# Optimization experiments

Measured on AMD Instinct MI355X. Metric: run time of the kernel, lower is better.

The kernel has to match this reference:

```python
import jax, jax.numpy as jnp
import numpy as np

N_NODES = 50000
N_EDGES = 800000
IN_FEAT = 128
HID = 128
OUT = 10
N_GRAPHS = 128
BN_EPS = 1e-5


def setup_inputs() -> dict:
    key = jax.random.key(0)
    ks = jax.random.split(key, 16)
    inp = {
        "n_feat": jax.random.normal(ks[0], (N_NODES, IN_FEAT), dtype=jnp.float32),
        "src": jax.random.randint(ks[1], (N_EDGES,), 0, N_NODES),
        "dst": jax.random.randint(ks[2], (N_EDGES,), 0, N_NODES),
        "graph_ids": jnp.sort(jax.random.randint(ks[3], (N_NODES,), 0, N_GRAPHS)),
        # GraphConv weights (DGL layout: weight [in, out], bias [out])
        "W1": jax.random.normal(ks[4], (IN_FEAT, HID), dtype=jnp.float32) / np.sqrt(IN_FEAT),
        "b1": jnp.zeros((HID,), dtype=jnp.float32),
        "W2": jax.random.normal(ks[5], (HID, HID), dtype=jnp.float32) / np.sqrt(HID),
        "b2": jnp.zeros((HID,), dtype=jnp.float32),
        # BatchNorm1d affine params
        "gamma": jnp.ones((HID,), dtype=jnp.float32),
        "beta": jnp.zeros((HID,), dtype=jnp.float32),
        # MLP head
        "fc1_w": jax.random.normal(ks[6], (HID, HID), dtype=jnp.float32) / np.sqrt(HID),
        "fc1_b": jnp.zeros((HID,), dtype=jnp.float32),
        "fc2_w": jax.random.normal(ks[7], (HID, OUT), dtype=jnp.float32) / np.sqrt(HID),
        "fc2_b": jnp.zeros((OUT,), dtype=jnp.float32),
    }
    return inp


def _graph_conv(x, W, b, src, dst, inv_sqrt_out, inv_sqrt_in):
    # DGL GraphConv, norm='both': h = D_in^{-1/2} A D_out^{-1/2} x W + b
    h = x * inv_sqrt_out[:, None]          # [N, d_in]
    h = h @ W                              # [N, d_out] (project before gather: fewer bytes moved)
    agg = jax.ops.segment_sum(h[src], dst, num_segments=N_NODES)  # gather + scatter-add
    return agg * inv_sqrt_in[:, None] + b


def reference(n_feat, src, dst, graph_ids, W1, b1, W2, b2, gamma, beta,
              fc1_w, fc1_b, fc2_w, fc2_b):
    ones_e = jnp.ones((N_EDGES,), dtype=jnp.float32)
    deg_out = jnp.clip(jax.ops.segment_sum(ones_e, src, num_segments=N_NODES), 1.0)
    deg_in = jnp.clip(jax.ops.segment_sum(ones_e, dst, num_segments=N_NODES), 1.0)
    inv_sqrt_out = jax.lax.rsqrt(deg_out)
    inv_sqrt_in = jax.lax.rsqrt(deg_in)

    x = jax.nn.relu(_graph_conv(n_feat, W1, b1, src, dst, inv_sqrt_out, inv_sqrt_in))
    # dropout is identity in eval mode
    x = jax.nn.relu(_graph_conv(x, W2, b2, src, dst, inv_sqrt_out, inv_sqrt_in))

    # SumPooling over graphs
    embedding = jax.ops.segment_sum(x, graph_ids, num_segments=N_GRAPHS)  # [B, HID]

    # BatchNorm1d (training-mode batch stats, biased variance like torch)
    mu = jnp.mean(embedding, axis=0)
    var = jnp.mean(jnp.square(embedding - mu), axis=0)
    h = gamma * (embedding - mu) * jax.lax.rsqrt(var + BN_EPS) + beta

    h = jax.nn.relu(h @ fc1_w + fc1_b)
    logits = h @ fc2_w + fc2_b
    return embedding, jax.nn.log_softmax(logits, axis=-1)
```

## Files before the change

kernel.cpp:

```cpp
#include <hip/hip_runtime.h>
#include <hip/hip_bf16.h>
#include <math.h>

#define N_NODES 50000
#define N_EDGES 800000
#define HID 128
#define N_GRAPHS 128
#define OUTC 10
#define BN_EPS 1e-5f

#define SCAN_B 256
#define N_SCAN_BLOCKS ((N_NODES + SCAN_B - 1) / SCAN_B)

#define HB 128
#define HW8 (N_NODES / 4)
#define HR_B 256
#define HR_BLOCKS ((HW8 + HR_B - 1) / HR_B)

#define EPAD 8
#define E_SRC_CAP (N_EDGES + N_NODES * EPAD)

#define LDA 136
#define LDAF 132

#define MM_BLOCKS ((N_NODES + 64) / 64)

#define AGG_NODES 16
#define AGG_BLOCKS (N_NODES / AGG_NODES)

#define PSLOTS 3

typedef short short8 __attribute__((ext_vector_type(8)));
typedef float floatx4 __attribute__((ext_vector_type(4)));

template <typename T, typename F>
__device__ inline T bitcast(F f) {
    union { F a; T b; } u;
    u.a = f;
    return u.b;
}

__device__ inline unsigned short f2bf(float x) {
    return __hip_bfloat16_raw(__float2bfloat16(x)).x;
}

__global__ __launch_bounds__(1024) void hist_part_kernel(const int* __restrict__ src,
                                                         const int* __restrict__ dst,
                                                         unsigned int* __restrict__ part,
                                                         const float* __restrict__ W1,
                                                         const float* __restrict__ W2,
                                                         unsigned short* __restrict__ Wp) {
    if (blockIdx.x == 2 * HB) {
        for (int q = threadIdx.x; q < 4096; q += 1024) {
            int wi = q >> 11;
            const float* __restrict__ W = wi ? W2 : W1;
            int t2 = q & 2047;
            int tile = t2 >> 6, lane = t2 & 63;
            int kc = tile >> 3, nt = tile & 7;
            int n = lane & 15, quad = lane >> 4;
            unsigned short v[8];
#pragma unroll
            for (int j = 0; j < 8; j++) {
                int k = kc * 32 + quad * 8 + j;
                v[j] = f2bf(W[k * HID + nt * 16 + n]);
            }
            *(uint4*)&Wp[(size_t)q * 8] = *(uint4*)v;
        }
        return;
    }
    __shared__ unsigned int h[HW8];
    for (int i = threadIdx.x; i < HW8; i += 1024) h[i] = 0;
    __syncthreads();
    int half = (blockIdx.x >= HB) ? 1 : 0;
    const int* __restrict__ idx = half ? dst : src;
    int b = blockIdx.x - half * HB;
    for (int e = b * 1024 + threadIdx.x; e < N_EDGES; e += HB * 1024) {
        int v = idx[e];
        atomicAdd(&h[v >> 2], 1u << ((v & 3) << 3));
    }
    __syncthreads();
    unsigned int* __restrict__ out = part + (size_t)blockIdx.x * HW8;
    for (int i = threadIdx.x; i < HW8; i += 1024) out[i] = h[i];
}

__global__ __launch_bounds__(HR_B) void hist_reduce_kernel(unsigned int* __restrict__ part,
                                                           int* __restrict__ cnt_in,
                                                           float* __restrict__ inv_out,
                                                           float* __restrict__ inv_in,
                                                           int* __restrict__ bsum) {
    int t = threadIdx.x;
    int w = blockIdx.x * HR_B + t;
    int padsum = 0;
    if (w < HW8) {
        unsigned int s = 0, d = 0;
        for (int b = 0; b < HB; b++) {
            s += part[(size_t)b * HW8 + w];
            unsigned int c = part[(size_t)(b + HB) * HW8 + w];
            part[(size_t)(b + HB) * HW8 + w] = d;
            d += c;
        }
#pragma unroll
        for (int j = 0; j < 4; j++) {
            int i = w * 4 + j;
            int so = (int)((s >> (j * 8)) & 0xFFu);
            int di = (int)((d >> (j * 8)) & 0xFFu);
            cnt_in[i] = di;
            inv_out[i] = rsqrtf(fmaxf((float)so, 1.0f));
            inv_in[i] = rsqrtf(fmaxf((float)di, 1.0f));
            padsum += (di + EPAD - 1) & ~(EPAD - 1);
        }
    }
#pragma unroll
    for (int o = 32; o > 0; o >>= 1) padsum += __shfl_xor(padsum, o);
    if ((t & 63) == 0) bsum[blockIdx.x * 4 + (t >> 6)] = padsum;
}

__device__ inline void mm_tail(const unsigned short* __restrict__ xs,
                               const unsigned short* __restrict__ Wp,
                               __hip_bfloat16* __restrict__ Y, int row0) {
    int tid = threadIdx.x;
    int wave = tid >> 6, lane = tid & 63;
    int m = lane & 15, quad = lane >> 4;
    int rowl = wave * 16;

    short8 a[4];
#pragma unroll
    for (int kc = 0; kc < 4; kc++)
        a[kc] = bitcast<short8>(*(const uint4*)&xs[(rowl + m) * LDA + kc * 32 + quad * 8]);

    floatx4 acc[8];
#pragma unroll
    for (int nt = 0; nt < 8; nt++) acc[nt] = (floatx4){0.f, 0.f, 0.f, 0.f};

#pragma unroll
    for (int nt = 0; nt < 8; nt++) {
#pragma unroll
        for (int kc = 0; kc < 4; kc++) {
            short8 bfr = bitcast<short8>(
                *(const uint4*)&Wp[((size_t)(kc * 8 + nt) * 64 + lane) * 8]);
            acc[nt] = __builtin_amdgcn_mfma_f32_16x16x32_bf16(a[kc], bfr, acc[nt], 0, 0, 0);
        }
    }

#pragma unroll
    for (int nt = 0; nt < 8; nt++) {
#pragma unroll
        for (int i = 0; i < 4; i++) {
            int rg = row0 + rowl + quad * 4 + i;
            if (rg < N_NODES + 1) {
                Y[(size_t)rg * HID + nt * 16 + m] = __float2bfloat16(acc[nt][i]);
            }
        }
    }
}

__global__ __launch_bounds__(256) void scanmm1_kernel(const int* __restrict__ cnt,
                                                      const int* __restrict__ bsum,
                                                      int* __restrict__ row_ptr,
                                                      int* __restrict__ edge_src,
                                                      const float* __restrict__ X,
                                                      const float* __restrict__ scale,
                                                      const unsigned short* __restrict__ Wp,
                                                      __hip_bfloat16* __restrict__ Y,
                                                      __hip_bfloat16* __restrict__ Y2,
                                                      float* __restrict__ emb) {
    __shared__ unsigned short xs[64 * LDA];
    int t = threadIdx.x;
    int b = blockIdx.x;

    if (b >= N_SCAN_BLOCKS) {
        if (b == N_SCAN_BLOCKS + MM_BLOCKS) {
            for (int i = t; i < N_GRAPHS * HID; i += 256) emb[i] = 0.f;
            if (t < 16) {
                uint4 z = make_uint4(0u, 0u, 0u, 0u);
                *(uint4*)&Y2[(size_t)N_NODES * HID + t * 8] = z;
            }
            return;
        }
        int row0 = (b - N_SCAN_BLOCKS) * 64;
        for (int j = 0; j < 8; j++) {
            int idx4 = j * 256 + t;
            int r = idx4 >> 5;
            int col = (idx4 & 31) * 4;
            int rg = row0 + r;
            float4 v = make_float4(0.f, 0.f, 0.f, 0.f);
            if (rg < N_NODES) {
                v = *(const float4*)&X[(size_t)rg * HID + col];
                float sc = scale[rg];
                v.x *= sc; v.y *= sc; v.z *= sc; v.w *= sc;
            }
            unsigned short o[4];
            o[0] = f2bf(v.x); o[1] = f2bf(v.y); o[2] = f2bf(v.z); o[3] = f2bf(v.w);
            *(ushort4*)&xs[r * LDA + col] = *(ushort4*)o;
        }
        __syncthreads();
        mm_tail(xs, Wp, Y, row0);
        return;
    }

    int* sb = (int*)xs;
    int* part = (int*)xs + 256;
    sb[t] = (t < N_SCAN_BLOCKS) ? bsum[t] : 0;
    __syncthreads();
    for (int off = 1; off < SCAN_B; off <<= 1) {
        int u = (t >= off) ? sb[t - off] : 0;
        __syncthreads();
        sb[t] += u;
        __syncthreads();
    }
    int boff = (b == 0) ? 0 : sb[b - 1];

    int i = b * SCAN_B + t;
    int raw = (i < N_NODES) ? cnt[i] : 0;
    int v = (raw + EPAD - 1) & ~(EPAD - 1);
    part[t] = v;
    __syncthreads();
    for (int off = 1; off < SCAN_B; off <<= 1) {
        int u = (t >= off) ? part[t - off] : 0;
        __syncthreads();
        part[t] += u;
        __syncthreads();
    }
    if (i < N_NODES) {
        int ex = part[t] - v + boff;
        row_ptr[i] = ex;
        for (int p = ex + raw; p < ex + v; p++) edge_src[p] = N_NODES;
        if (i == N_NODES - 1) row_ptr[N_NODES] = ex + v;
    }
}

__global__ __launch_bounds__(1024) void csr_fill_kernel(const int* __restrict__ src,
                                                        const int* __restrict__ dst,
                                                        const unsigned int* __restrict__ part,
                                                        const int* __restrict__ row_ptr,
                                                        int* __restrict__ edge_src) {
    __shared__ unsigned int loc[HW8];
    int b = blockIdx.x;
    const unsigned int* __restrict__ off = part + (size_t)(b + HB) * HW8;
    for (int i = threadIdx.x; i < HW8; i += 1024) loc[i] = off[i];
    __syncthreads();
    for (int e = b * 1024 + threadIdx.x; e < N_EDGES; e += HB * 1024) {
        int d = dst[e];
        unsigned int old = atomicAdd(&loc[d >> 2], 1u << ((d & 3) << 3));
        int local = (int)((old >> ((d & 3) << 3)) & 0xFFu);
        edge_src[row_ptr[d] + local] = src[e];
    }
}

#define ACC8(u)                                                                              \
    acc[0] += __uint_as_float(u.x << 16); acc[1] += __uint_as_float(u.x & 0xFFFF0000u);      \
    acc[2] += __uint_as_float(u.y << 16); acc[3] += __uint_as_float(u.y & 0xFFFF0000u);      \
    acc[4] += __uint_as_float(u.z << 16); acc[5] += __uint_as_float(u.z & 0xFFFF0000u);      \
    acc[6] += __uint_as_float(u.w << 16); acc[7] += __uint_as_float(u.w & 0xFFFF0000u);

#define GATHER_CONT(idxv)                                                                    \
    for (int j = 16; j < mm0; j += 8) {                                                      \
        int s0 = __shfl(idxv, j + esub);                                                     \
        int s1 = __shfl(idxv, j + 4 + esub);                                                 \
        uint4 u0 = Yq[s0 * (HID / 8) + f16];                                                 \
        uint4 u1 = Yq[s1 * (HID / 8) + f16];                                                 \
        ACC8(u0); ACC8(u1);                                                                  \
    }

#define GATHER_BODY(idxv)                                                                    \
    {                                                                                        \
        int j = 0;                                                                           \
        for (; j + 16 <= mm; j += 16) {                                                      \
            int s0 = __shfl(idxv, j + esub);                                                 \
            int s1 = __shfl(idxv, j + 4 + esub);                                             \
            int s2 = __shfl(idxv, j + 8 + esub);                                             \
            int s3 = __shfl(idxv, j + 12 + esub);                                            \
            uint4 u0 = Yq[s0 * (HID / 8) + f16];                                             \
            uint4 u1 = Yq[s1 * (HID / 8) + f16];                                             \
            uint4 u2 = Yq[s2 * (HID / 8) + f16];                                             \
            uint4 u3 = Yq[s3 * (HID / 8) + f16];                                             \
            ACC8(u0); ACC8(u1); ACC8(u2); ACC8(u3);                                          \
        }                                                                                    \
        if (j < mm) {                                                                        \
            int s0 = __shfl(idxv, j + esub);                                                 \
            int s1 = __shfl(idxv, j + 4 + esub);                                             \
            uint4 u0 = Yq[s0 * (HID / 8) + f16];                                             \
            uint4 u1 = Yq[s1 * (HID / 8) + f16];                                             \
            ACC8(u0); ACC8(u1);                                                              \
        }                                                                                    \
    }

#define GATHER_PREAMBLE(nbexpr)                                                              \
    int nb = (nbexpr);                                                                       \
    int begs[4], ends[4], idx0[4];                                                           \
    _Pragma("unroll") for (int it = 0; it < 4; it++) {                                       \
        begs[it] = row_ptr[nb + it];                                                         \
        ends[it] = row_ptr[nb + it + 1];                                                     \
    }                                                                                        \
    _Pragma("unroll") for (int it = 0; it < 4; it++) {                                       \
        int mmw = min(64, ends[it] - begs[it]);                                              \
        idx0[it] = (lane < mmw) ? edge_src[begs[it] + lane] : N_NODES;                       \
    }                                                                                        \
    uint4 pf[4][4];                                                                          \
    _Pragma("unroll") for (int it = 0; it < 4; it++) {                                       \
        int s0 = __shfl(idx0[it], esub);                                                     \
        int s1 = __shfl(idx0[it], 4 + esub);                                                 \
        int s2 = __shfl(idx0[it], 8 + esub);                                                 \
        int s3 = __shfl(idx0[it], 12 + esub);                                                \
        pf[it][0] = Yq[s0 * (HID / 8) + f16];                                                \
        pf[it][1] = Yq[s1 * (HID / 8) + f16];                                                \
        pf[it][2] = Yq[s2 * (HID / 8) + f16];                                                \
        pf[it][3] = Yq[s3 * (HID / 8) + f16];                                                \
    }

#define GATHER_NODE(it)                                                                      \
    float acc[8] = {};                                                                       \
    ACC8(pf[it][0]); ACC8(pf[it][1]); ACC8(pf[it][2]); ACC8(pf[it][3]);                      \
    int mm0 = min(64, ends[it] - begs[it]);                                                  \
    GATHER_CONT(idx0[it]);                                                                   \
    for (int base = begs[it] + 64; base < ends[it]; base += 64) {                            \
        int mm = min(64, ends[it] - base);                                                   \
        int idx = (lane < mm) ? edge_src[base + lane] : N_NODES;                             \
        GATHER_BODY(idx);                                                                    \
    }

__global__ __launch_bounds__(256) void agg1mm2_kernel(const __hip_bfloat16* __restrict__ Y1,
                                                      const int* __restrict__ edge_src,
                                                      const int* __restrict__ row_ptr,
                                                      const float* __restrict__ inv_in,
                                                      const float* __restrict__ inv_out,
                                                      const float* __restrict__ bias,
                                                      const unsigned short* __restrict__ Wp2,
                                                      __hip_bfloat16* __restrict__ Y2) {
    __shared__ unsigned short xs[AGG_NODES * LDA];
    const uint4* __restrict__ Yq = (const uint4*)Y1;
    int wave = threadIdx.x >> 6;
    int lane = threadIdx.x & 63;
    int esub = lane >> 4;
    int f16 = lane & 15;

    GATHER_PREAMBLE(blockIdx.x * AGG_NODES + wave * 4)

#pragma unroll
    for (int it = 0; it < 4; it++) {
        GATHER_NODE(it)
#pragma unroll
        for (int i = 0; i < 8; i++) {
            acc[i] += __shfl_xor(acc[i], 16);
            acc[i] += __shfl_xor(acc[i], 32);
        }
        if (lane < 16) {
            int n = nb + it;
            float si = inv_in[n];
            float so = inv_out[n];
            int f0 = f16 * 8;
            float4 b0 = *(const float4*)&bias[f0];
            float4 b1 = *(const float4*)&bias[f0 + 4];
            unsigned short u[8];
            u[0] = f2bf(fmaxf(acc[0] * si + b0.x, 0.f) * so);
            u[1] = f2bf(fmaxf(acc[1] * si + b0.y, 0.f) * so);
            u[2] = f2bf(fmaxf(acc[2] * si + b0.z, 0.f) * so);
            u[3] = f2bf(fmaxf(acc[3] * si + b0.w, 0.f) * so);
            u[4] = f2bf(fmaxf(acc[4] * si + b1.x, 0.f) * so);
            u[5] = f2bf(fmaxf(acc[5] * si + b1.y, 0.f) * so);
            u[6] = f2bf(fmaxf(acc[6] * si + b1.z, 0.f) * so);
            u[7] = f2bf(fmaxf(acc[7] * si + b1.w, 0.f) * so);
            *(uint4*)&xs[(wave * 4 + it) * LDA + f0] = *(uint4*)u;
        }
    }
    __syncthreads();

    int m = lane & 15, quad = lane >> 4;
    short8 a[4];
#pragma unroll
    for (int kc = 0; kc < 4; kc++)
        a[kc] = bitcast<short8>(*(const uint4*)&xs[m * LDA + kc * 32 + quad * 8]);
#pragma unroll
    for (int w2 = 0; w2 < 2; w2++) {
        int nt = wave * 2 + w2;
        floatx4 acc2 = (floatx4){0.f, 0.f, 0.f, 0.f};
#pragma unroll
        for (int kc = 0; kc < 4; kc++) {
            short8 bfr = bitcast<short8>(
                *(const uint4*)&Wp2[((size_t)(kc * 8 + nt) * 64 + lane) * 8]);
            acc2 = __builtin_amdgcn_mfma_f32_16x16x32_bf16(a[kc], bfr, acc2, 0, 0, 0);
        }
#pragma unroll
        for (int i = 0; i < 4; i++) {
            int rg = blockIdx.x * AGG_NODES + quad * 4 + i;
            Y2[(size_t)rg * HID + nt * 16 + m] = __float2bfloat16(acc2[i]);
        }
    }
}

__global__ __launch_bounds__(256) void agg2pool_kernel(const __hip_bfloat16* __restrict__ Y,
                                                       const int* __restrict__ edge_src,
                                                       const int* __restrict__ row_ptr,
                                                       const float* __restrict__ inv_in,
                                                       const float* __restrict__ bias,
                                                       const int* __restrict__ gid,
                                                       float* __restrict__ pe,
                                                       int* __restrict__ ptag,
                                                       float* __restrict__ emb) {
    __shared__ float xp[AGG_NODES * LDAF];
    __shared__ int gl[AGG_NODES];
    const uint4* __restrict__ Yq = (const uint4*)Y;
    int t = threadIdx.x;
    int wave = t >> 6;
    int lane = t & 63;
    int esub = lane >> 4;
    int f16 = lane & 15;
    int nb0 = blockIdx.x * AGG_NODES;

    if (t < AGG_NODES) gl[t] = gid[nb0 + t];

    GATHER_PREAMBLE(nb0 + wave * 4)

#pragma unroll
    for (int it = 0; it < 4; it++) {
        GATHER_NODE(it)
#pragma unroll
        for (int i = 0; i < 8; i++) {
            acc[i] += __shfl_xor(acc[i], 16);
            acc[i] += __shfl_xor(acc[i], 32);
        }
        if (lane < 16) {
            int n = nb + it;
            float si = inv_in[n];
            int f0 = f16 * 8;
            float4 b0 = *(const float4*)&bias[f0];
            float4 b1 = *(const float4*)&bias[f0 + 4];
            float4 o0, o1;
            o0.x = fmaxf(acc[0] * si + b0.x, 0.f);
            o0.y = fmaxf(acc[1] * si + b0.y, 0.f);
            o0.z = fmaxf(acc[2] * si + b0.z, 0.f);
            o0.w = fmaxf(acc[3] * si + b0.w, 0.f);
            o1.x = fmaxf(acc[4] * si + b1.x, 0.f);
            o1.y = fmaxf(acc[5] * si + b1.y, 0.f);
            o1.z = fmaxf(acc[6] * si + b1.z, 0.f);
            o1.w = fmaxf(acc[7] * si + b1.w, 0.f);
            *(float4*)&xp[(wave * 4 + it) * LDAF + f0] = o0;
            *(float4*)&xp[(wave * 4 + it) * LDAF + f0 + 4] = o1;
        }
    }
    __syncthreads();

    if (t < HID) {
        int f = t;
        int r = 0;
        int g = gl[0];
        float run = 0.f;
#pragma unroll
        for (int k = 0; k < AGG_NODES; k++) {
            int gk = gl[k];
            if (gk != g) {
                if (r < PSLOTS) {
                    pe[((size_t)blockIdx.x * PSLOTS + r) * HID + f] = run;
                    if (f == 0) ptag[blockIdx.x * PSLOTS + r] = g;
                } else {
                    atomicAdd(&emb[g * HID + f], run);
                }
                r++;
                g = gk;
                run = 0.f;
            }
            run += xp[k * LDAF + f];
        }
        if (r < PSLOTS) {
            pe[((size_t)blockIdx.x * PSLOTS + r) * HID + f] = run;
            if (f == 0) ptag[blockIdx.x * PSLOTS + r] = g;
        } else {
            atomicAdd(&emb[g * HID + f], run);
        }
        r++;
        if (f == 0) {
            for (; r < PSLOTS; r++) ptag[blockIdx.x * PSLOTS + r] = -1;
        }
    }
}

__global__ __launch_bounds__(HID) void pool_reduce_kernel(const float* __restrict__ pe,
                                                          const int* __restrict__ ptag,
                                                          const int* __restrict__ gid,
                                                          float* __restrict__ emb) {
    int g = blockIdx.x, f = threadIdx.x;
    __shared__ int bounds[2];
    if (f == 0) {
        int lo = 0, hi = N_NODES;
        while (lo < hi) { int mid = (lo + hi) >> 1; if (gid[mid] < g) lo = mid + 1; else hi = mid; }
        bounds[0] = lo;
        hi = N_NODES;
        while (lo < hi) { int mid = (lo + hi) >> 1; if (gid[mid] <= g) lo = mid + 1; else hi = mid; }
        bounds[1] = lo;
    }
    __syncthreads();
    int n0 = bounds[0], n1 = bounds[1];
    float acc = emb[g * HID + f];
    if (n0 < n1) {
        int b0 = n0 >> 4, b1 = (n1 - 1) >> 4;
        for (int b = b0; b <= b1; b++) {
#pragma unroll
            for (int r = 0; r < PSLOTS; r++) {
                if (ptag[b * PSLOTS + r] == g) acc += pe[((size_t)b * PSLOTS + r) * HID + f];
            }
        }
    }
    emb[g * HID + f] = acc;
}

__global__ __launch_bounds__(128) void head_fused_kernel(const float* __restrict__ emb,
                                                         const float* __restrict__ gamma,
                                                         const float* __restrict__ beta,
                                                         const float* __restrict__ fc1_w,
                                                         const float* __restrict__ fc1_b,
                                                         const float* __restrict__ fc2_w,
                                                         const float* __restrict__ fc2_b,
                                                         float* __restrict__ out) {
    int r = blockIdx.x, f = threadIdx.x;
    float s = 0.f;
    for (int row = 0; row < N_GRAPHS; row++) s += emb[row * HID + f];
    float mu = s * (1.f / N_GRAPHS);
    float v = 0.f;
    for (int row = 0; row < N_GRAPHS; row++) {
        float d = emb[row * HID + f] - mu;
        v += d * d;
    }
    v *= (1.f / N_GRAPHS);
    float sc = gamma[f] * rsqrtf(v + BN_EPS);
    float sh = beta[f] - mu * sc;

    __shared__ float xr[HID];
    xr[f] = emb[r * HID + f] * sc + sh;
    __syncthreads();
    float acc = fc1_b[f];
    for (int k = 0; k < HID; k++) acc += xr[k] * fc1_w[k * HID + f];
    __shared__ float hr[HID];
    hr[f] = fmaxf(acc, 0.f);
    __syncthreads();

    __shared__ float logits[OUTC];
    __shared__ float mstat[2];
    if (f < OUTC) {
        float a = fc2_b[f];
        for (int k = 0; k < HID; k++) a += hr[k] * fc2_w[k * OUTC + f];
        logits[f] = a;
    }
    __syncthreads();
    if (f == 0) {
        float m = logits[0];
        for (int o = 1; o < OUTC; o++) m = fmaxf(m, logits[o]);
        float sum = 0.f;
        for (int o = 0; o < OUTC; o++) sum += expf(logits[o] - m);
        mstat[0] = m;
        mstat[1] = logf(sum);
    }
    __syncthreads();
    if (f < OUTC) out[r * OUTC + f] = logits[f] - mstat[0] - mstat[1];
}

extern "C" void kernel_launch(void* const* d_in, const int* in_sizes, int n_in,
                              void* d_out, int out_size, void* d_ws, size_t ws_size,
                              hipStream_t stream) {
    const float* n_feat = (const float*)d_in[0];
    const int*   src    = (const int*)d_in[1];
    const int*   dst    = (const int*)d_in[2];
    const int*   gid    = (const int*)d_in[3];
    const float* W1     = (const float*)d_in[4];
    const float* b1     = (const float*)d_in[5];
    const float* W2     = (const float*)d_in[6];
    const float* b2     = (const float*)d_in[7];
    const float* gamma  = (const float*)d_in[8];
    const float* beta   = (const float*)d_in[9];
    const float* fc1_w  = (const float*)d_in[10];
    const float* fc1_b  = (const float*)d_in[11];
    const float* fc2_w  = (const float*)d_in[12];
    const float* fc2_b  = (const float*)d_in[13];

    char* wsb = (char*)d_ws;
    size_t off = 0;
    auto alloc = [&](size_t bytes) -> void* {
        void* p = wsb + off;
        off += (bytes + 255) & ~(size_t)255;
        return p;
    };
    int*   cnt_in  = (int*)alloc((size_t)N_NODES * 4);
    int*   row_ptr = (int*)alloc((size_t)(N_NODES + 1) * 4);
    int*   e_src   = (int*)alloc((size_t)E_SRC_CAP * 4);
    float* inv_out = (float*)alloc((size_t)N_NODES * 4);
    float* inv_in  = (float*)alloc((size_t)N_NODES * 4);
    unsigned int* part = (unsigned int*)alloc((size_t)2 * HB * HW8 * 4);
    __hip_bfloat16* Y1 = (__hip_bfloat16*)alloc((size_t)(N_NODES + 1) * HID * 2);
    __hip_bfloat16* Y2 = (__hip_bfloat16*)alloc((size_t)(N_NODES + 1) * HID * 2);
    float* pe      = (float*)alloc((size_t)AGG_BLOCKS * PSLOTS * HID * 4);
    int*   ptag    = (int*)alloc((size_t)AGG_BLOCKS * PSLOTS * 4);
    unsigned short* Wp = (unsigned short*)alloc((size_t)2 * 32 * 64 * 8 * 2);
    int*   bsum    = (int*)alloc((size_t)SCAN_B * 4);

    float* emb_out = (float*)d_out;
    float* lsm_out = emb_out + N_GRAPHS * HID;

    hist_part_kernel<<<2 * HB + 1, 1024, 0, stream>>>(src, dst, part, W1, W2, Wp);
    hist_reduce_kernel<<<HR_BLOCKS, HR_B, 0, stream>>>(part, cnt_in, inv_out, inv_in, bsum);
    scanmm1_kernel<<<N_SCAN_BLOCKS + MM_BLOCKS + 1, 256, 0, stream>>>(
        cnt_in, bsum, row_ptr, e_src, n_feat, inv_out, Wp, Y1, Y2, emb_out);
    csr_fill_kernel<<<HB, 1024, 0, stream>>>(src, dst, part, row_ptr, e_src);

    agg1mm2_kernel<<<AGG_BLOCKS, 256, 0, stream>>>(Y1, e_src, row_ptr, inv_in, inv_out,
                                                   b1, Wp + (size_t)32 * 64 * 8, Y2);
    agg2pool_kernel<<<AGG_BLOCKS, 256, 0, stream>>>(Y2, e_src, row_ptr, inv_in, b2, gid,
                                                    pe, ptag, emb_out);
    pool_reduce_kernel<<<N_GRAPHS, HID, 0, stream>>>(pe, ptag, gid, emb_out);
    head_fused_kernel<<<N_GRAPHS, HID, 0, stream>>>(emb_out, gamma, beta, fc1_w, fc1_b,
                                                    fc2_w, fc2_b, lsm_out);
}
```

Baseline: 243.5 us.

## Split second aggregation+pooling kernel across feature halves to double blocks

The layer-2 aggregation/pooling kernel now launches twice as many blocks, each handling one 64-feature half of the 128-wide rows. Eight lanes cover a half-row, so each wave gathers eight edges at once, and the first loads for all four nodes are issued before any accumulation. The aim is more parallelism and more memory-level parallelism in the gather. In exchange, edge indices and row pointers are read twice, and each half-block does its own pooling writes to separate feature ranges.

```diff
diff --git a/kernel.cpp b/kernel.cpp
--- a/kernel.cpp
+++ b/kernel.cpp
@@ -21,7 +21,7 @@
 #define E_SRC_CAP (N_EDGES + N_NODES * EPAD)
 
 #define LDA 136
-#define LDAF 132
+#define LDAF2 68
 
 #define MM_BLOCKS ((N_NODES + 64) / 64)
 
@@ -397,34 +397,73 @@
                                                        float* __restrict__ pe,
                                                        int* __restrict__ ptag,
                                                        float* __restrict__ emb) {
-    __shared__ float xp[AGG_NODES * LDAF];
+    __shared__ float xp[AGG_NODES * LDAF2];
     __shared__ int gl[AGG_NODES];
-    const uint4* __restrict__ Yq = (const uint4*)Y;
+    int half = (blockIdx.x >= AGG_BLOCKS) ? 1 : 0;
+    int blk = blockIdx.x - half * AGG_BLOCKS;
+    const uint4* __restrict__ Yq = (const uint4*)Y + half * 8;
     int t = threadIdx.x;
     int wave = t >> 6;
     int lane = t & 63;
-    int esub = lane >> 4;
-    int f16 = lane & 15;
-    int nb0 = blockIdx.x * AGG_NODES;
+    int esub = lane >> 3;
+    int f8 = lane & 7;
+    int nb0 = blk * AGG_NODES;
+    int nb = nb0 + wave * 4;
 
     if (t < AGG_NODES) gl[t] = gid[nb0 + t];
 
-    GATHER_PREAMBLE(nb0 + wave * 4)
-
+    int begs[4], ends[4], idx0[4];
 #pragma unroll
     for (int it = 0; it < 4; it++) {
-        GATHER_NODE(it)
+        begs[it] = row_ptr[nb + it];
+        ends[it] = row_ptr[nb + it + 1];
+    }
+#pragma unroll
+    for (int it = 0; it < 4; it++) {
+        int mmw = min(64, ends[it] - begs[it]);
+        idx0[it] = (lane < mmw) ? edge_src[begs[it] + lane] : N_NODES;
+    }
+    uint4 pf[4][2];
+#pragma unroll
+    for (int it = 0; it < 4; it++) {
+        int s0 = __shfl(idx0[it], esub);
+        int s1 = __shfl(idx0[it], 8 + esub);
+        pf[it][0] = Yq[s0 * (HID / 8) + f8];
+        pf[it][1] = Yq[s1 * (HID / 8) + f8];
+    }
+
+#pragma unroll
+    for (int it = 0; it < 4; it++) {
+        float acc[8] = {};
+        ACC8(pf[it][0]);
+        ACC8(pf[it][1]);
+        int mm0 = min(64, ends[it] - begs[it]);
+        for (int j = 16; j < mm0; j += 8) {
+            int s = __shfl(idx0[it], j + esub);
+            uint4 u = Yq[s * (HID / 8) + f8];
+            ACC8(u);
+        }
+        for (int base = begs[it] + 64; base < ends[it]; base += 64) {
+            int mm = min(64, ends[it] - base);
+            int idx = (lane < mm) ? edge_src[base + lane] : N_NODES;
+            for (int j = 0; j < mm; j += 8) {
+                int s = __shfl(idx, j + esub);
+                uint4 u = Yq[s * (HID / 8) + f8];
+                ACC8(u);
+            }
+        }
 #pragma unroll
         for (int i = 0; i < 8; i++) {
+            acc[i] += __shfl_xor(acc[i], 8);
             acc[i] += __shfl_xor(acc[i], 16);
             acc[i] += __shfl_xor(acc[i], 32);
         }
-        if (lane < 16) {
+        if (lane < 8) {
             int n = nb + it;
             float si = inv_in[n];
-            int f0 = f16 * 8;
-            float4 b0 = *(const float4*)&bias[f0];
-            float4 b1 = *(const float4*)&bias[f0 + 4];
+            int fg0 = half * 64 + f8 * 8;
+            float4 b0 = *(const float4*)&bias[fg0];
+            float4 b1 = *(const float4*)&bias[fg0 + 4];
             float4 o0, o1;
             o0.x = fmaxf(acc[0] * si + b0.x, 0.f);
             o0.y = fmaxf(acc[1] * si + b0.y, 0.f);
@@ -434,14 +473,15 @@
             o1.y = fmaxf(acc[5] * si + b1.y, 0.f);
             o1.z = fmaxf(acc[6] * si + b1.z, 0.f);
             o1.w = fmaxf(acc[7] * si + b1.w, 0.f);
-            *(float4*)&xp[(wave * 4 + it) * LDAF + f0] = o0;
-            *(float4*)&xp[(wave * 4 + it) * LDAF + f0 + 4] = o1;
-        }
-    }
-    __syncthreads();
-
-    if (t < HID) {
+            *(float4*)&xp[(wave * 4 + it) * LDAF2 + f8 * 8] = o0;
+            *(float4*)&xp[(wave * 4 + it) * LDAF2 + f8 * 8 + 4] = o1;
+        }
+    }
+    __syncthreads();
+
+    if (t < 64) {
         int f = t;
+        int fg = half * 64 + t;
         int r = 0;
         int g = gl[0];
         float run = 0.f;
@@ -450,26 +490,26 @@
             int gk = gl[k];
             if (gk != g) {
                 if (r < PSLOTS) {
-                    pe[((size_t)blockIdx.x * PSLOTS + r) * HID + f] = run;
-                    if (f == 0) ptag[blockIdx.x * PSLOTS + r] = g;
+                    pe[((size_t)blk * PSLOTS + r) * HID + fg] = run;
+                    if (half == 0 && f == 0) ptag[blk * PSLOTS + r] = g;
                 } else {
-                    atomicAdd(&emb[g * HID + f], run);
+                    atomicAdd(&emb[g * HID + fg], run);
                 }
                 r++;
                 g = gk;
                 run = 0.f;
             }
-            run += xp[k * LDAF + f];
+            run += xp[k * LDAF2 + f];
         }
         if (r < PSLOTS) {
-            pe[((size_t)blockIdx.x * PSLOTS + r) * HID + f] = run;
-            if (f == 0) ptag[blockIdx.x * PSLOTS + r] = g;
+            pe[((size_t)blk * PSLOTS + r) * HID + fg] = run;
+            if (half == 0 && f == 0) ptag[blk * PSLOTS + r] = g;
         } else {
-            atomicAdd(&emb[g * HID + f], run);
+            atomicAdd(&emb[g * HID + fg], run);
         }
         r++;
-        if (f == 0) {
-            for (; r < PSLOTS; r++) ptag[blockIdx.x * PSLOTS + r] = -1;
+        if (half == 0 && f == 0) {
+            for (; r < PSLOTS; r++) ptag[blk * PSLOTS + r] = -1;
         }
     }
 }
@@ -602,8 +642,8 @@
 
     agg1mm2_kernel<<<AGG_BLOCKS, 256, 0, stream>>>(Y1, e_src, row_ptr, inv_in, inv_out,
                                                    b1, Wp + (size_t)32 * 64 * 8, Y2);
-    agg2pool_kernel<<<AGG_BLOCKS, 256, 0, stream>>>(Y2, e_src, row_ptr, inv_in, b2, gid,
-                                                    pe, ptag, emb_out);
+    agg2pool_kernel<<<2 * AGG_BLOCKS, 256, 0, stream>>>(Y2, e_src, row_ptr, inv_in, b2, gid,
+                                                        pe, ptag, emb_out);
     pool_reduce_kernel<<<N_GRAPHS, HID, 0, stream>>>(pe, ptag, gid, emb_out);
     head_fused_kernel<<<N_GRAPHS, HID, 0, stream>>>(emb_out, gamma, beta, fc1_w, fc1_b,
                                                     fc2_w, fc2_b, lsm_out);
```

Result: slower. 249.4 us (+2.4%).
